# Performance work log

Hardware: AMD Instinct MI355X
Metric: run time of the kernel (lower is better)

The kernel has to match this reference:

```python
import jax, jax.numpy as jnp
import numpy as np

B, T, H, P, N = 32, 512, 128, 16, 16
D = 4 * H


def _lstm(x, Wih, Whh, bih, bhh):
    # standard torch-style LSTM, batch_first input x: [B, T, 1], zero init state
    Bz = x.shape[0]
    Hh = Whh.shape[1]
    h0 = jnp.zeros((Bz, Hh), x.dtype)

    def step(carry, xt):
        h, c = carry
        g = xt @ Wih.T + bih + h @ Whh.T + bhh  # [B, 4H], gate order i,f,g,o
        i, f, gg, o = jnp.split(g, 4, axis=-1)
        c = jax.nn.sigmoid(f) * c + jax.nn.sigmoid(i) * jnp.tanh(gg)
        h = jax.nn.sigmoid(o) * jnp.tanh(c)
        return (h, c), h

    _, hs = jax.lax.scan(step, (h0, h0), jnp.swapaxes(x, 0, 1))
    return jnp.swapaxes(hs, 0, 1)  # [B, T, H]


def _forward(Y, Xp, Xn, Xi, init_c, init_h, Wih, Whh, bih, bhh,
             Wc, Uc, bc, Wg, Ug, bg, Wf, Uf, bf, Wo, Uo, bo, Wa,
             Watt, batt, vatt, W1, b1, W2, b2, W3, b3):
    run = lambda x: _lstm(x, Wih, Whh, bih, bhh)
    Y1 = run(Y)                                              # [B,T,H]
    Xi1 = run(Xi)
    Xp1 = jnp.mean(jax.vmap(run)(jnp.moveaxis(Xp, 1, 0)), axis=0)  # mean over P stocks
    Xn1 = jnp.mean(jax.vmap(run)(jnp.moveaxis(Xn, 1, 0)), axis=0)
    result = jnp.concatenate([Y1, Xp1, Xn1, Xi1], axis=2)    # [B,T,4H]

    Hh = Wa.shape[0]

    def mi_step(carry, xt):  # Mi-LSTM cell: 4 input streams with gated-candidate attention
        c, h = carry
        xs = xt.reshape(xt.shape[0], 4, Hh)                  # split 4H into 4 streams
        cand = jnp.tanh(jnp.einsum('bkh,khj->bkj', xs, Wc) + jnp.einsum('bh,khj->bkj', h, Uc) + bc)
        ig = jax.nn.sigmoid(jnp.einsum('bkh,khj->bkj', xs, Wg) + jnp.einsum('bh,khj->bkj', h, Ug) + bg)
        l = ig * cand                                        # [B,4,H]
        a = jax.nn.softmax(jnp.einsum('bkj,bj->bk', l, c @ Wa), axis=1)
        lmix = jnp.einsum('bk,bkj->bj', a, l)
        f = jax.nn.sigmoid(xt @ Wf + h @ Uf + bf)
        o = jax.nn.sigmoid(xt @ Wo + h @ Uo + bo)
        c = f * c + lmix
        h = o * jnp.tanh(c)
        return (c, h), h

    _, hs = jax.lax.scan(mi_step, (init_c, init_h), jnp.swapaxes(result, 0, 1))
    Y2 = jnp.swapaxes(hs, 0, 1)                              # [B,T,H]

    # temporal attention over the Mi-LSTM outputs
    scores = jnp.tanh(Y2 @ Watt + batt) @ vatt               # [B,T]
    attw = jax.nn.softmax(scores, axis=1)
    Y3 = jnp.einsum('bt,bth->bh', attw, Y2)                  # [B,H]

    hm = jax.nn.relu(Y3 @ W1 + b1)
    hm = jax.nn.relu(hm @ W2 + b2)
    return hm @ W3 + b3                                      # [B,1]


def setup_inputs() -> dict:
    key = jax.random.key(0)
    ks = jax.random.split(key, 24)
    u = lambda k, s: jax.random.uniform(k, s, dtype=jnp.float32)
    nr = lambda k, s: jax.random.normal(k, s, dtype=jnp.float32) * 0.05
    z = lambda s: jnp.zeros(s, jnp.float32)
    return {
        'Y': u(ks[0], (B, T, 1)), 'Xp': u(ks[1], (B, P, T, 1)), 'Xn': u(ks[2], (B, N, T, 1)),
        'Xi': u(ks[3], (B, T, 1)), 'Target': u(ks[4], (B, 1)),
        'init_c': u(ks[5], (B, H)), 'init_h': u(ks[6], (B, H)),
        'Wih': nr(ks[7], (4 * H, 1)), 'Whh': nr(ks[8], (4 * H, H)), 'bih': z(4 * H), 'bhh': z(4 * H),
        'Wc': nr(ks[9], (4, H, H)), 'Uc': nr(ks[10], (4, H, H)), 'bc': z((4, H)),
        'Wg': nr(ks[11], (4, H, H)), 'Ug': nr(ks[12], (4, H, H)), 'bg': z((4, H)),
        'Wf': nr(ks[13], (D, H)), 'Uf': nr(ks[14], (H, H)), 'bf': z(H),
        'Wo': nr(ks[15], (D, H)), 'Uo': nr(ks[16], (H, H)), 'bo': z(H),
        'Wa': nr(ks[17], (H, H)),
        'Watt': nr(ks[18], (H, H)), 'batt': z(H), 'vatt': nr(ks[19], (H,)),
        'W1': nr(ks[20], (H, H)), 'b1': z(H),
        'W2': nr(ks[21], (H, H)), 'b2': z(H),
        'W3': nr(ks[22], (H, 1)), 'b3': z(1),
    }


def reference(Y, Xp, Xn, Xi, Target, init_c, init_h, Wih, Whh, bih, bhh,
              Wc, Uc, bc, Wg, Ug, bg, Wf, Uf, bf, Wo, Uo, bo, Wa,
              Watt, batt, vatt, W1, b1, W2, b2, W3, b3):
    out = _forward(Y, Xp, Xn, Xi, init_c, init_h, Wih, Whh, bih, bhh,
                   Wc, Uc, bc, Wg, Ug, bg, Wf, Uf, bf, Wo, Uo, bo, Wa,
                   Watt, batt, vatt, W1, b1, W2, b2, W3, b3)
    loss = jnp.mean((out - Target) ** 2)
    return out, loss
```

## Files before the change

kernel.cpp:

```cpp
#include <hip/hip_runtime.h>
#include <hip/hip_fp16.h>

typedef _Float16 half8 __attribute__((ext_vector_type(8)));
typedef float float4_ __attribute__((ext_vector_type(4)));

__device__ __forceinline__ float rcp_(float x) { return __builtin_amdgcn_rcpf(x); }
__device__ __forceinline__ float sigf(float x) { return rcp_(1.f + __expf(-x)); }
__device__ __forceinline__ float tanhf2(float x) {
  x = fminf(fmaxf(x, -15.f), 15.f);
  float e = __expf(-2.f * x);
  return (1.f - e) * rcp_(1.f + e);
}

__global__ __launch_bounds__(512, 2)
void k1_lstm(const float* __restrict__ Y, const float* __restrict__ Xp,
             const float* __restrict__ Xn, const float* __restrict__ Xi,
             const float* __restrict__ Wih, const float* __restrict__ Whh,
             const float* __restrict__ bih, const float* __restrict__ bhh,
             _Float16* __restrict__ result)
{
  __shared__ float x_lds[16][513];
  __shared__ _Float16 hbuf[2][16][136];

  const int tid  = threadIdx.x;
  const int wv   = tid >> 6;
  const int lane = tid & 63;
  const int cl   = lane & 15;
  const int rowg = lane >> 4;
  const int bid  = blockIdx.x;

  const float* xsrc; int slot; int do_mean; int b_out_base;
  if (bid < 2)       { xsrc = Y  + (size_t)(bid * 16) * 512;        slot = 0; do_mean = 0; b_out_base = bid * 16; }
  else if (bid < 4)  { xsrc = Xi + (size_t)((bid - 2) * 16) * 512;  slot = 3; do_mean = 0; b_out_base = (bid - 2) * 16; }
  else if (bid < 36) { xsrc = Xp + (size_t)((bid - 4) * 16) * 512;  slot = 1; do_mean = 1; b_out_base = bid - 4; }
  else               { xsrc = Xn + (size_t)((bid - 36) * 16) * 512; slot = 2; do_mean = 1; b_out_base = bid - 36; }

  for (int i = tid; i < 16 * 512; i += 512) {
    int r = i >> 9, t = i & 511;
    x_lds[r][t] = xsrc[r * 512 + t];
  }
  for (int i = tid; i < 16 * 136; i += 512) {
    hbuf[0][i / 136][i % 136] = (_Float16)0.f;
  }

  const int cg = wv * 16 + cl;
  half8 bw[4][4];
  #pragma unroll
  for (int g = 0; g < 4; ++g) {
    #pragma unroll
    for (int kc = 0; kc < 4; ++kc) {
      const float* p = Whh + (size_t)(g * 128 + cg) * 128 + kc * 32 + rowg * 8;
      half8 v;
      #pragma unroll
      for (int j = 0; j < 8; ++j) v[j] = (_Float16)p[j];
      bw[g][kc] = v;
    }
  }
  float wih_r[4], bias_r[4];
  #pragma unroll
  for (int g = 0; g < 4; ++g) {
    wih_r[g]  = Wih[g * 128 + cg];
    bias_r[g] = bih[g * 128 + cg] + bhh[g * 128 + cg];
  }

  float c_reg[4] = {0.f, 0.f, 0.f, 0.f};
  float hvp[4] = {0.f, 0.f, 0.f, 0.f};
  float sprev = 0.f;
  __syncthreads();

  for (int t = 0; t < 512; ++t) {
    if (t > 0) {
      if (!do_mean) {
        #pragma unroll
        for (int i = 0; i < 4; ++i) {
          int b = b_out_base + rowg * 4 + i;
          result[(((size_t)b * 512 + (t - 1)) * 4 + slot) * 128 + cg] = (_Float16)hvp[i];
        }
      } else {
        if (rowg == 0)
          result[(((size_t)b_out_base * 512 + (t - 1)) * 4 + slot) * 128 + cg] = (_Float16)sprev;
      }
    }

    const int cur = t & 1;
    half8 a[4];
    #pragma unroll
    for (int kc = 0; kc < 4; ++kc)
      a[kc] = *(const half8*)&hbuf[cur][cl][kc * 32 + rowg * 8];

    float4_ acc[4];
    #pragma unroll
    for (int g = 0; g < 4; ++g) {
      float4_ z = {0.f, 0.f, 0.f, 0.f};
      #pragma unroll
      for (int kc = 0; kc < 4; ++kc)
        z = __builtin_amdgcn_mfma_f32_16x16x32_f16(a[kc], bw[g][kc], z, 0, 0, 0);
      acc[g] = z;
    }

    float hv[4];
    #pragma unroll
    for (int i = 0; i < 4; ++i) {
      const int row = rowg * 4 + i;
      float x  = x_lds[row][t];
      float ui = acc[0][i] + x * wih_r[0] + bias_r[0];
      float uf = acc[1][i] + x * wih_r[1] + bias_r[1];
      float ug = acc[2][i] + x * wih_r[2] + bias_r[2];
      float uo = acc[3][i] + x * wih_r[3] + bias_r[3];
      float ii = sigf(ui), ff = sigf(uf), gg = tanhf2(ug), oo = sigf(uo);
      float c  = ff * c_reg[i] + ii * gg;
      c_reg[i] = c;
      float h  = oo * tanhf2(c);
      hv[i] = h;
      hbuf[cur ^ 1][row][cg] = (_Float16)h;
    }

    if (!do_mean) {
      #pragma unroll
      for (int i = 0; i < 4; ++i) hvp[i] = hv[i];
    } else {
      float s = hv[0] + hv[1] + hv[2] + hv[3];
      s += __shfl_xor(s, 16, 64);
      s += __shfl_xor(s, 32, 64);
      sprev = s * 0.0625f;
    }
    __syncthreads();
  }

  if (!do_mean) {
    #pragma unroll
    for (int i = 0; i < 4; ++i) {
      int b = b_out_base + rowg * 4 + i;
      result[(((size_t)b * 512 + 511) * 4 + slot) * 128 + cg] = (_Float16)hvp[i];
    }
  } else {
    if (rowg == 0)
      result[(((size_t)b_out_base * 512 + 511) * 4 + slot) * 128 + cg] = (_Float16)sprev;
  }
}

__global__ __launch_bounds__(512, 2)
void k2_gemm(const _Float16* __restrict__ result,
             const float* __restrict__ Wc, const float* __restrict__ Wg,
             const float* __restrict__ Wf, const float* __restrict__ Wo,
             _Float16* __restrict__ candX, _Float16* __restrict__ igX,
             _Float16* __restrict__ fX, _Float16* __restrict__ oX)
{
  __shared__ _Float16 a_lds[128][136];
  __shared__ _Float16 bt_lds[256][136];

  const int tid   = threadIdx.x;
  const int lane  = tid & 63;
  const int wv    = tid >> 6;
  const int cl    = lane & 15, rowg = lane >> 4;
  const int mtile = blockIdx.x;
  const int role  = blockIdx.y;

  const int nchunks = (role == 0) ? 4 : 1;
  const int kstream = role - 1;

  float4_ acc[16];
  #pragma unroll
  for (int n = 0; n < 16; ++n) acc[n] = (float4_){0.f, 0.f, 0.f, 0.f};

  for (int ch = 0; ch < nchunks; ++ch) {
    const int koff = (role == 0) ? ch * 128 : kstream * 128;
    for (int i = tid; i < 1024; i += 512) {
      int r = i >> 3, v8 = i & 7;
      half8 val = *(const half8*)&result[((size_t)(mtile * 128 + r)) * 512 + koff + v8 * 8];
      *(half8*)&a_lds[r][v8 * 8] = val;
    }
    for (int i = tid; i < 128 * 256; i += 512) {
      int n = i & 255, kk = i >> 8;
      float w;
      if (role == 0) {
        w = (n < 128) ? Wf[(size_t)(ch * 128 + kk) * 128 + n]
                      : Wo[(size_t)(ch * 128 + kk) * 128 + (n - 128)];
      } else {
        w = (n < 128) ? Wc[(size_t)(kstream * 128 + kk) * 128 + n]
                      : Wg[(size_t)(kstream * 128 + kk) * 128 + (n - 128)];
      }
      bt_lds[n][kk] = (_Float16)w;
    }
    __syncthreads();
    #pragma unroll
    for (int kc = 0; kc < 4; ++kc) {
      half8 a = *(const half8*)&a_lds[wv * 16 + cl][kc * 32 + rowg * 8];
      #pragma unroll
      for (int n = 0; n < 16; ++n) {
        half8 bb = *(const half8*)&bt_lds[n * 16 + cl][kc * 32 + rowg * 8];
        acc[n] = __builtin_amdgcn_mfma_f32_16x16x32_f16(a, bb, acc[n], 0, 0, 0);
      }
    }
    __syncthreads();
  }

  #pragma unroll
  for (int n = 0; n < 16; ++n) {
    int col = n * 16 + cl;
    #pragma unroll
    for (int i = 0; i < 4; ++i) {
      size_t r = (size_t)mtile * 128 + wv * 16 + rowg * 4 + i;
      _Float16 v = (_Float16)acc[n][i];
      if (role == 0) {
        if (col < 128) fX[r * 128 + col] = v;
        else           oX[r * 128 + (col - 128)] = v;
      } else {
        if (col < 128) candX[(r * 4 + kstream) * 128 + col] = v;
        else           igX  [(r * 4 + kstream) * 128 + (col - 128)] = v;
      }
    }
  }
}

__global__ __launch_bounds__(512, 1)
void k3_scan(const float* __restrict__ Uc, const float* __restrict__ Ug,
             const float* __restrict__ Uf, const float* __restrict__ Uo,
             const float* __restrict__ Wa,
             const float* __restrict__ bc, const float* __restrict__ bg,
             const float* __restrict__ bfv, const float* __restrict__ bov,
             const float* __restrict__ init_c, const float* __restrict__ init_h,
             const _Float16* __restrict__ candX, const _Float16* __restrict__ igX,
             const _Float16* __restrict__ fX, const _Float16* __restrict__ oX,
             _Float16* __restrict__ Y2)
{
  __shared__ __align__(16) unsigned h_pk[64];
  __shared__ __align__(16) unsigned c_pk[64];
  __shared__ float c_f32[128];
  __shared__ __align__(16) float raw[1408];
  __shared__ float part2[2][4];
  __shared__ __align__(16) _Float16 in_c[16 * 512];
  __shared__ __align__(16) _Float16 in_g[16 * 512];
  __shared__ __align__(16) _Float16 in_f[16 * 128];
  __shared__ __align__(16) _Float16 in_o[16 * 128];
  __shared__ __align__(16) _Float16 y2s[16 * 128];

  const int tid  = threadIdx.x;
  const int b    = blockIdx.x;
  const int wv   = tid >> 6;
  const int lane = tid & 63;
  const int cl   = lane & 15;
  const int rowg = lane >> 4;

  half8 wfrag[11][4];
  #pragma unroll
  for (int gi = 0; gi < 11; ++gi) {
    const int col = (wv * 11 + gi) * 16 + cl;
    const float* src;
    if (col < 512)       src = Uc + (col >> 7) * 16384 + (col & 127);
    else if (col < 1024) src = Ug + ((col >> 7) - 4) * 16384 + (col & 127);
    else if (col < 1152) src = Uf + (col - 1024);
    else if (col < 1280) src = Uo + (col - 1152);
    else                 src = Wa + (col - 1280);
    #pragma unroll
    for (int kc = 0; kc < 4; ++kc) {
      half8 v;
      #pragma unroll
      for (int j = 0; j < 8; ++j)
        v[j] = (_Float16)src[(kc * 32 + rowg * 8 + j) * 128];
      wfrag[gi][kc] = v;
    }
  }

  float bc_r[4] = {0, 0, 0, 0}, bg_r[4] = {0, 0, 0, 0}, bf_r = 0.f, bo_r = 0.f;
  if (tid < 128) {
    #pragma unroll
    for (int k = 0; k < 4; ++k) { bc_r[k] = bc[k * 128 + tid]; bg_r[k] = bg[k * 128 + tid]; }
    bf_r = bfv[tid]; bo_r = bov[tid];
    c_f32[tid] = init_c[b * 128 + tid];
  }
  if (tid < 64) {
    union { _Float16 h[2]; unsigned u; } hp, cp;
    hp.h[0] = (_Float16)init_h[b * 128 + 2 * tid];
    hp.h[1] = (_Float16)init_h[b * 128 + 2 * tid + 1];
    cp.h[0] = (_Float16)init_c[b * 128 + 2 * tid];
    cp.h[1] = (_Float16)init_c[b * 128 + 2 * tid + 1];
    h_pk[tid] = hp.u;
    c_pk[tid] = cp.u;
  }
  __syncthreads();

  uint4* y2g = (uint4*)Y2;

  for (int chunk = 0; chunk < 32; ++chunk) {
    if (chunk > 0 && tid < 256)
      y2g[(size_t)b * 8192 + (size_t)(chunk - 1) * 256 + tid] = ((const uint4*)y2s)[tid];
    {
      const uint4* c4 = (const uint4*)(candX + ((size_t)b * 512 + chunk * 16) * 512);
      const uint4* g4 = (const uint4*)(igX   + ((size_t)b * 512 + chunk * 16) * 512);
      ((uint4*)in_c)[tid]       = c4[tid];
      ((uint4*)in_c)[tid + 512] = c4[tid + 512];
      ((uint4*)in_g)[tid]       = g4[tid];
      ((uint4*)in_g)[tid + 512] = g4[tid + 512];
      if (tid < 256)
        ((uint4*)in_f)[tid] = ((const uint4*)(fX + ((size_t)b * 512 + chunk * 16) * 128))[tid];
      else
        ((uint4*)in_o)[tid - 256] = ((const uint4*)(oX + ((size_t)b * 512 + chunk * 16) * 128))[tid - 256];
    }
    __syncthreads();

    for (int s = 0; s < 16; ++s) {
      float cx[4] = {0, 0, 0, 0}, gx[4] = {0, 0, 0, 0}, fx = 0.f, ox = 0.f;
      if (tid < 128) {
        #pragma unroll
        for (int k = 0; k < 4; ++k) {
          cx[k] = (float)in_c[(s * 4 + k) * 128 + tid];
          gx[k] = (float)in_g[(s * 4 + k) * 128 + tid];
        }
        fx = (float)in_f[s * 128 + tid];
        ox = (float)in_o[s * 128 + tid];
      }

      {
        const uint4* hp4 = (const uint4*)h_pk;
        const uint4* cp4 = (const uint4*)c_pk;
        union { uint4 u; half8 h; } hb[4], cb[4];
        #pragma unroll
        for (int kc = 0; kc < 4; ++kc) {
          hb[kc].u = hp4[kc * 4 + rowg];
          cb[kc].u = cp4[kc * 4 + rowg];
        }
        #pragma unroll
        for (int gi = 0; gi < 11; ++gi) {
          const int g = wv * 11 + gi;
          float4_ acc = {0.f, 0.f, 0.f, 0.f};
          if (g < 80) {
            #pragma unroll
            for (int kc = 0; kc < 4; ++kc)
              acc = __builtin_amdgcn_mfma_f32_16x16x32_f16(wfrag[gi][kc], hb[kc].h, acc, 0, 0, 0);
          } else {
            #pragma unroll
            for (int kc = 0; kc < 4; ++kc)
              acc = __builtin_amdgcn_mfma_f32_16x16x32_f16(wfrag[gi][kc], cb[kc].h, acc, 0, 0, 0);
          }
          if (cl == 0)
            *(float4_*)&raw[g * 16 + rowg * 4] = acc;
        }
      }
      __syncthreads();

      float l0 = 0.f, l1 = 0.f, l2 = 0.f, l3 = 0.f, fj = 0.f, oj = 0.f;
      if (tid < 128) {
        float cand[4], ig[4];
        #pragma unroll
        for (int k = 0; k < 4; ++k) {
          float uc = cx[k] + raw[k * 128 + tid] + bc_r[k];
          float ui = gx[k] + raw[512 + k * 128 + tid] + bg_r[k];
          cand[k] = tanhf2(uc);
          ig[k]   = sigf(ui);
        }
        l0 = ig[0] * cand[0]; l1 = ig[1] * cand[1];
        l2 = ig[2] * cand[2]; l3 = ig[3] * cand[3];
        float cwa = raw[1280 + tid];
        float p0 = l0 * cwa, p1 = l1 * cwa, p2 = l2 * cwa, p3 = l3 * cwa;
        #pragma unroll
        for (int m = 1; m < 64; m <<= 1) {
          p0 += __shfl_xor(p0, m, 64);
          p1 += __shfl_xor(p1, m, 64);
          p2 += __shfl_xor(p2, m, 64);
          p3 += __shfl_xor(p3, m, 64);
        }
        if ((tid & 63) == 0) {
          part2[tid >> 6][0] = p0; part2[tid >> 6][1] = p1;
          part2[tid >> 6][2] = p2; part2[tid >> 6][3] = p3;
        }
        fj = sigf(fx + raw[1024 + tid] + bf_r);
        oj = sigf(ox + raw[1152 + tid] + bo_r);
      }
      __syncthreads();

      if (tid < 128) {
        float d0 = part2[0][0] + part2[1][0];
        float d1 = part2[0][1] + part2[1][1];
        float d2 = part2[0][2] + part2[1][2];
        float d3 = part2[0][3] + part2[1][3];
        float mx = fmaxf(fmaxf(d0, d1), fmaxf(d2, d3));
        float e0 = __expf(d0 - mx), e1 = __expf(d1 - mx);
        float e2 = __expf(d2 - mx), e3 = __expf(d3 - mx);
        float inv = rcp_(e0 + e1 + e2 + e3);
        float lmix = (e0 * l0 + e1 * l1 + e2 * l2 + e3 * l3) * inv;
        float c = fj * c_f32[tid] + lmix;
        c_f32[tid] = c;
        float h = oj * tanhf2(c);
        ((_Float16*)h_pk)[tid] = (_Float16)h;
        ((_Float16*)c_pk)[tid] = (_Float16)c;
        y2s[s * 128 + tid] = (_Float16)h;
      }
      __syncthreads();
    }
  }

  if (tid < 256)
    y2g[(size_t)b * 8192 + (size_t)31 * 256 + tid] = ((const uint4*)y2s)[tid];
}

__global__ __launch_bounds__(256, 1)
void k4_attn(const _Float16* __restrict__ Y2,
             const float* __restrict__ Watt, const float* __restrict__ batt,
             const float* __restrict__ vatt,
             const float* __restrict__ W1, const float* __restrict__ b1,
             const float* __restrict__ W2, const float* __restrict__ b2,
             const float* __restrict__ W3, const float* __restrict__ b3,
             float* __restrict__ out)
{
  __shared__ _Float16 wt_lds[128][136];
  __shared__ float sc[512];
  __shared__ float red[8];
  __shared__ float y3[128];
  __shared__ float hm[128];

  const int tid = threadIdx.x;
  const int b   = blockIdx.x;
  const int lane = tid & 63, wv = tid >> 6;
  const int cl = lane & 15, rowg = lane >> 4;

  for (int i = tid; i < 128 * 128; i += 256) {
    int h = i >> 7, j = i & 127;
    wt_lds[j][h] = (_Float16)Watt[h * 128 + j];
  }
  __syncthreads();

  half8 bw[8][4];
  #pragma unroll
  for (int n = 0; n < 8; ++n)
    #pragma unroll
    for (int kc = 0; kc < 4; ++kc)
      bw[n][kc] = *(const half8*)&wt_lds[n * 16 + cl][kc * 32 + rowg * 8];
  float battr[8], vattr[8];
  #pragma unroll
  for (int n = 0; n < 8; ++n) { battr[n] = batt[n * 16 + cl]; vattr[n] = vatt[n * 16 + cl]; }

  for (int mt = wv * 8; mt < wv * 8 + 8; ++mt) {
    half8 a[4];
    #pragma unroll
    for (int kc = 0; kc < 4; ++kc)
      a[kc] = *(const half8*)&Y2[((size_t)b * 512 + mt * 16 + cl) * 128 + kc * 32 + rowg * 8];
    float sp[4] = {0.f, 0.f, 0.f, 0.f};
    #pragma unroll
    for (int n = 0; n < 8; ++n) {
      float4_ acc = {0.f, 0.f, 0.f, 0.f};
      #pragma unroll
      for (int kc = 0; kc < 4; ++kc)
        acc = __builtin_amdgcn_mfma_f32_16x16x32_f16(a[kc], bw[n][kc], acc, 0, 0, 0);
      #pragma unroll
      for (int i = 0; i < 4; ++i)
        sp[i] += tanhf2(acc[i] + battr[n]) * vattr[n];
    }
    #pragma unroll
    for (int i = 0; i < 4; ++i) {
      #pragma unroll
      for (int m = 1; m < 16; m <<= 1) sp[i] += __shfl_xor(sp[i], m, 64);
    }
    if (cl == 0) {
      #pragma unroll
      for (int i = 0; i < 4; ++i) sc[mt * 16 + rowg * 4 + i] = sp[i];
    }
  }
  __syncthreads();

  float v0 = sc[tid], v1 = sc[tid + 256];
  float mx = fmaxf(v0, v1);
  #pragma unroll
  for (int m = 1; m < 64; m <<= 1) mx = fmaxf(mx, __shfl_xor(mx, m, 64));
  if (lane == 0) red[wv] = mx;
  __syncthreads();
  mx = fmaxf(fmaxf(red[0], red[1]), fmaxf(red[2], red[3]));
  float e0 = __expf(v0 - mx), e1 = __expf(v1 - mx);
  float s = e0 + e1;
  #pragma unroll
  for (int m = 1; m < 64; m <<= 1) s += __shfl_xor(s, m, 64);
  __syncthreads();
  if (lane == 0) red[wv] = s;
  __syncthreads();
  float inv = rcp_(red[0] + red[1] + red[2] + red[3]);
  sc[tid] = e0 * inv;
  sc[tid + 256] = e1 * inv;
  __syncthreads();

  {
    int h = tid & 127, part = tid >> 7;
    float acc = 0.f;
    for (int t = part * 256; t < part * 256 + 256; ++t)
      acc += sc[t] * (float)Y2[((size_t)b * 512 + t) * 128 + h];
    if (part == 0) y3[h] = acc;
    __syncthreads();
    if (part == 1) y3[h] += acc;
    __syncthreads();
  }

  if (tid < 128) {
    float a1 = 0.f;
    for (int h2 = 0; h2 < 128; ++h2) a1 += y3[h2] * W1[h2 * 128 + tid];
    hm[tid] = fmaxf(a1 + b1[tid], 0.f);
  }
  __syncthreads();
  if (tid < 128) {
    float a2 = 0.f;
    for (int h2 = 0; h2 < 128; ++h2) a2 += hm[h2] * W2[h2 * 128 + tid];
    a2 = fmaxf(a2 + b2[tid], 0.f);
    float p = a2 * W3[tid];
    #pragma unroll
    for (int m = 1; m < 64; m <<= 1) p += __shfl_xor(p, m, 64);
    if ((tid & 63) == 0) red[4 + (tid >> 6)] = p;
  }
  __syncthreads();
  if (tid == 0) out[b] = red[4] + red[5] + b3[0];
}

__global__ void k5_loss(const float* __restrict__ out, const float* __restrict__ target,
                        float* __restrict__ loss_out)
{
  int l = threadIdx.x;
  float v = 0.f;
  if (l < 32) { float d = out[l] - target[l]; v = d * d; }
  #pragma unroll
  for (int m = 1; m < 64; m <<= 1) v += __shfl_xor(v, m, 64);
  if (l == 0) loss_out[0] = v * (1.f / 32.f);
}

extern "C" void kernel_launch(void* const* d_in, const int* in_sizes, int n_in,
                              void* d_out, int out_size, void* d_ws, size_t ws_size,
                              hipStream_t stream)
{
  const float* Y      = (const float*)d_in[0];
  const float* Xp     = (const float*)d_in[1];
  const float* Xn     = (const float*)d_in[2];
  const float* Xi     = (const float*)d_in[3];
  const float* Target = (const float*)d_in[4];
  const float* init_c = (const float*)d_in[5];
  const float* init_h = (const float*)d_in[6];
  const float* Wih    = (const float*)d_in[7];
  const float* Whh    = (const float*)d_in[8];
  const float* bih    = (const float*)d_in[9];
  const float* bhh    = (const float*)d_in[10];
  const float* Wc     = (const float*)d_in[11];
  const float* Uc     = (const float*)d_in[12];
  const float* bc     = (const float*)d_in[13];
  const float* Wg     = (const float*)d_in[14];
  const float* Ug     = (const float*)d_in[15];
  const float* bg     = (const float*)d_in[16];
  const float* Wf     = (const float*)d_in[17];
  const float* Uf     = (const float*)d_in[18];
  const float* bf     = (const float*)d_in[19];
  const float* Wo     = (const float*)d_in[20];
  const float* Uo     = (const float*)d_in[21];
  const float* bo     = (const float*)d_in[22];
  const float* Wa     = (const float*)d_in[23];
  const float* Watt   = (const float*)d_in[24];
  const float* batt   = (const float*)d_in[25];
  const float* vatt   = (const float*)d_in[26];
  const float* W1     = (const float*)d_in[27];
  const float* b1     = (const float*)d_in[28];
  const float* W2     = (const float*)d_in[29];
  const float* b2     = (const float*)d_in[30];
  const float* W3     = (const float*)d_in[31];
  const float* b3     = (const float*)d_in[32];

  char* ws = (char*)d_ws;
  _Float16* result = (_Float16*)(ws);
  _Float16* candX  = (_Float16*)(ws + ((size_t)16 << 20));
  _Float16* igX    = (_Float16*)(ws + ((size_t)32 << 20));
  _Float16* fXp    = (_Float16*)(ws + ((size_t)48 << 20));
  _Float16* oXp    = (_Float16*)(ws + ((size_t)52 << 20));
  _Float16* Y2     = (_Float16*)(ws + ((size_t)56 << 20));
  float* outp = (float*)d_out;

  k1_lstm<<<dim3(68), dim3(512), 0, stream>>>(Y, Xp, Xn, Xi, Wih, Whh, bih, bhh, result);
  k2_gemm<<<dim3(128, 5), dim3(512), 0, stream>>>(result, Wc, Wg, Wf, Wo, candX, igX, fXp, oXp);
  k3_scan<<<dim3(32), dim3(512), 0, stream>>>(Uc, Ug, Uf, Uo, Wa, bc, bg, bf, bo,
                                              init_c, init_h, candX, igX, fXp, oXp, Y2);
  k4_attn<<<dim3(32), dim3(256), 0, stream>>>(Y2, Watt, batt, vatt, W1, b1, W2, b2, W3, b3, outp);
  k5_loss<<<dim3(1), dim3(64), 0, stream>>>(outp, Target, outp + 32);
}
```

Before: 1.801 ms.

## Run Mi-LSTM pointwise step in one wavefront, two hidden units per lane

The per-step elementwise stage of the Mi-LSTM scan now runs in a single 64-lane wavefront, with each lane handling two hidden units. The attention dot products then reduce entirely within that wavefront. This removes the cross-wave partial-sum buffer and one block-wide barrier per timestep, and it keeps the cell state in registers instead of LDS. In exchange each lane does twice the transcendental work, so the serial critical path per step may get longer.

Result: no change. 1.772 ms (-1.6%).

```diff
diff --git a/kernel.cpp b/kernel.cpp
--- a/kernel.cpp
+++ b/kernel.cpp
@@ -10,6 +10,10 @@
   x = fminf(fmaxf(x, -15.f), 15.f);
   float e = __expf(-2.f * x);
   return (1.f - e) * rcp_(1.f + e);
+}
+__device__ __forceinline__ float2 up2(unsigned u) {
+  union { unsigned u; _Float16 h[2]; } cv; cv.u = u;
+  return make_float2((float)cv.h[0], (float)cv.h[1]);
 }
 
 __global__ __launch_bounds__(512, 2)
@@ -226,9 +230,7 @@
 {
   __shared__ __align__(16) unsigned h_pk[64];
   __shared__ __align__(16) unsigned c_pk[64];
-  __shared__ float c_f32[128];
   __shared__ __align__(16) float raw[1408];
-  __shared__ float part2[2][4];
   __shared__ __align__(16) _Float16 in_c[16 * 512];
   __shared__ __align__(16) _Float16 in_g[16 * 512];
   __shared__ __align__(16) _Float16 in_f[16 * 128];
@@ -262,21 +264,23 @@
     }
   }
 
-  float bc_r[4] = {0, 0, 0, 0}, bg_r[4] = {0, 0, 0, 0}, bf_r = 0.f, bo_r = 0.f;
-  if (tid < 128) {
-    #pragma unroll
-    for (int k = 0; k < 4; ++k) { bc_r[k] = bc[k * 128 + tid]; bg_r[k] = bg[k * 128 + tid]; }
-    bf_r = bfv[tid]; bo_r = bov[tid];
-    c_f32[tid] = init_c[b * 128 + tid];
-  }
+  float c0 = 0.f, c1 = 0.f;
+  float2 bc2[4], bg2[4], bf2 = {0.f, 0.f}, bo2 = {0.f, 0.f};
   if (tid < 64) {
-    union { _Float16 h[2]; unsigned u; } hp, cp;
-    hp.h[0] = (_Float16)init_h[b * 128 + 2 * tid];
-    hp.h[1] = (_Float16)init_h[b * 128 + 2 * tid + 1];
-    cp.h[0] = (_Float16)init_c[b * 128 + 2 * tid];
-    cp.h[1] = (_Float16)init_c[b * 128 + 2 * tid + 1];
-    h_pk[tid] = hp.u;
-    c_pk[tid] = cp.u;
+    float2 ci = *(const float2*)&init_c[b * 128 + 2 * tid];
+    float2 hi = *(const float2*)&init_h[b * 128 + 2 * tid];
+    c0 = ci.x; c1 = ci.y;
+    union { _Float16 h[2]; unsigned u; } hu, cu;
+    hu.h[0] = (_Float16)hi.x; hu.h[1] = (_Float16)hi.y;
+    cu.h[0] = (_Float16)ci.x; cu.h[1] = (_Float16)ci.y;
+    h_pk[tid] = hu.u; c_pk[tid] = cu.u;
+    #pragma unroll
+    for (int k = 0; k < 4; ++k) {
+      bc2[k] = *(const float2*)&bc[k * 128 + 2 * tid];
+      bg2[k] = *(const float2*)&bg[k * 128 + 2 * tid];
+    }
+    bf2 = *(const float2*)&bfv[2 * tid];
+    bo2 = *(const float2*)&bov[2 * tid];
   }
   __syncthreads();
 
@@ -300,17 +304,6 @@
     __syncthreads();
 
     for (int s = 0; s < 16; ++s) {
-      float cx[4] = {0, 0, 0, 0}, gx[4] = {0, 0, 0, 0}, fx = 0.f, ox = 0.f;
-      if (tid < 128) {
-        #pragma unroll
-        for (int k = 0; k < 4; ++k) {
-          cx[k] = (float)in_c[(s * 4 + k) * 128 + tid];
-          gx[k] = (float)in_g[(s * 4 + k) * 128 + tid];
-        }
-        fx = (float)in_f[s * 128 + tid];
-        ox = (float)in_o[s * 128 + tid];
-      }
-
       {
         const uint4* hp4 = (const uint4*)h_pk;
         const uint4* cp4 = (const uint4*)c_pk;
@@ -339,52 +332,56 @@
       }
       __syncthreads();
 
-      float l0 = 0.f, l1 = 0.f, l2 = 0.f, l3 = 0.f, fj = 0.f, oj = 0.f;
-      if (tid < 128) {
-        float cand[4], ig[4];
+      if (tid < 64) {
+        float2 cxv[4], gxv[4];
         #pragma unroll
         for (int k = 0; k < 4; ++k) {
-          float uc = cx[k] + raw[k * 128 + tid] + bc_r[k];
-          float ui = gx[k] + raw[512 + k * 128 + tid] + bg_r[k];
-          cand[k] = tanhf2(uc);
-          ig[k]   = sigf(ui);
+          cxv[k] = up2(((const unsigned*)in_c)[(s * 4 + k) * 64 + tid]);
+          gxv[k] = up2(((const unsigned*)in_g)[(s * 4 + k) * 64 + tid]);
         }
-        l0 = ig[0] * cand[0]; l1 = ig[1] * cand[1];
-        l2 = ig[2] * cand[2]; l3 = ig[3] * cand[3];
-        float cwa = raw[1280 + tid];
-        float p0 = l0 * cwa, p1 = l1 * cwa, p2 = l2 * cwa, p3 = l3 * cwa;
+        float2 fxv = up2(((const unsigned*)in_f)[s * 64 + tid]);
+        float2 oxv = up2(((const unsigned*)in_o)[s * 64 + tid]);
+
+        float2 cwa = *(const float2*)&raw[1280 + 2 * tid];
+        float l0[4], l1[4], p[4];
+        #pragma unroll
+        for (int k = 0; k < 4; ++k) {
+          float2 rc = *(const float2*)&raw[k * 128 + 2 * tid];
+          float2 rg = *(const float2*)&raw[512 + k * 128 + 2 * tid];
+          float ca0 = tanhf2(cxv[k].x + rc.x + bc2[k].x);
+          float ca1 = tanhf2(cxv[k].y + rc.y + bc2[k].y);
+          float g0  = sigf(gxv[k].x + rg.x + bg2[k].x);
+          float g1  = sigf(gxv[k].y + rg.y + bg2[k].y);
+          l0[k] = g0 * ca0; l1[k] = g1 * ca1;
+          p[k]  = l0[k] * cwa.x + l1[k] * cwa.y;
+        }
+        float2 rf = *(const float2*)&raw[1024 + 2 * tid];
+        float2 ro = *(const float2*)&raw[1152 + 2 * tid];
+        float f0 = sigf(fxv.x + rf.x + bf2.x), f1 = sigf(fxv.y + rf.y + bf2.y);
+        float o0 = sigf(oxv.x + ro.x + bo2.x), o1 = sigf(oxv.y + ro.y + bo2.y);
+
         #pragma unroll
         for (int m = 1; m < 64; m <<= 1) {
-          p0 += __shfl_xor(p0, m, 64);
-          p1 += __shfl_xor(p1, m, 64);
-          p2 += __shfl_xor(p2, m, 64);
-          p3 += __shfl_xor(p3, m, 64);
+          p[0] += __shfl_xor(p[0], m, 64);
+          p[1] += __shfl_xor(p[1], m, 64);
+          p[2] += __shfl_xor(p[2], m, 64);
+          p[3] += __shfl_xor(p[3], m, 64);
         }
-        if ((tid & 63) == 0) {
-          part2[tid >> 6][0] = p0; part2[tid >> 6][1] = p1;
-          part2[tid >> 6][2] = p2; part2[tid >> 6][3] = p3;
-        }
-        fj = sigf(fx + raw[1024 + tid] + bf_r);
-        oj = sigf(ox + raw[1152 + tid] + bo_r);
-      }
-      __syncthreads();
-
-      if (tid < 128) {
-        float d0 = part2[0][0] + part2[1][0];
-        float d1 = part2[0][1] + part2[1][1];
-        float d2 = part2[0][2] + part2[1][2];
-        float d3 = part2[0][3] + part2[1][3];
-        float mx = fmaxf(fmaxf(d0, d1), fmaxf(d2, d3));
-        float e0 = __expf(d0 - mx), e1 = __expf(d1 - mx);
-        float e2 = __expf(d2 - mx), e3 = __expf(d3 - mx);
+        float mx = fmaxf(fmaxf(p[0], p[1]), fmaxf(p[2], p[3]));
+        float e0 = __expf(p[0] - mx), e1 = __expf(p[1] - mx);
+        float e2 = __expf(p[2] - mx), e3 = __expf(p[3] - mx);
         float inv = rcp_(e0 + e1 + e2 + e3);
-        float lmix = (e0 * l0 + e1 * l1 + e2 * l2 + e3 * l3) * inv;
-        float c = fj * c_f32[tid] + lmix;
-        c_f32[tid] = c;
-        float h = oj * tanhf2(c);
-        ((_Float16*)h_pk)[tid] = (_Float16)h;
-        ((_Float16*)c_pk)[tid] = (_Float16)c;
-        y2s[s * 128 + tid] = (_Float16)h;
+        float lm0 = (e0 * l0[0] + e1 * l0[1] + e2 * l0[2] + e3 * l0[3]) * inv;
+        float lm1 = (e0 * l1[0] + e1 * l1[1] + e2 * l1[2] + e3 * l1[3]) * inv;
+        c0 = f0 * c0 + lm0;
+        c1 = f1 * c1 + lm1;
+        float h0 = o0 * tanhf2(c0), h1 = o1 * tanhf2(c1);
+        union { _Float16 h[2]; unsigned u; } hu, cu;
+        hu.h[0] = (_Float16)h0; hu.h[1] = (_Float16)h1;
+        cu.h[0] = (_Float16)c0; cu.h[1] = (_Float16)c1;
+        h_pk[tid] = hu.u;
+        c_pk[tid] = cu.u;
+        ((unsigned*)y2s)[s * 64 + tid] = hu.u;
       }
       __syncthreads();
     }
```
